# Optimization experiments

Measured on AMD Instinct MI355X. Metric: run time of the kernel, lower is better.

## Reference

```python
import jax, jax.numpy as jnp
import numpy as np

EMBED_DIM = 512
NUM_HEADS = 64
HEAD_DIM = EMBED_DIM // NUM_HEADS  # 8 quantum wires per head
BATCH = 4
SEQ = 1024


def setup_inputs() -> dict:
    key = jax.random.key(0)
    ks = jax.random.split(key, 5)
    s = 1.0 / np.sqrt(EMBED_DIM)
    x = jax.random.normal(ks[0], (BATCH, SEQ, EMBED_DIM), dtype=jnp.float32)
    Wqkv = jax.random.normal(ks[1], (3 * EMBED_DIM, EMBED_DIM), dtype=jnp.float32) * s
    Wout = jax.random.normal(ks[2], (EMBED_DIM, EMBED_DIM), dtype=jnp.float32) * s
    bout = jax.random.normal(ks[3], (EMBED_DIM,), dtype=jnp.float32) * 0.01
    # trainable RX angles, one per (head, wire)
    theta = jax.random.uniform(ks[4], (NUM_HEADS, HEAD_DIM), dtype=jnp.float32,
                               minval=-np.pi, maxval=np.pi)
    return {"x": x, "Wqkv": Wqkv, "Wout": Wout, "bout": bout, "theta": theta}


def _quantum_heads(t, theta):
    # t: [B, H, S, D]; theta: [H, D]
    # Circuit per head: RX(t_i) then RX(theta_i) on wire i (angles add),
    # CNOT chain 0->1->...->D-1, then <Z_j>.
    # Heisenberg: Z_j -> Z_0...Z_j, so <Z_j> = prod_{i<=j} cos(t_i + theta_i).
    c = jnp.cos(t + theta[None, :, None, :])
    return jnp.cumprod(c, axis=-1)


def reference(x, Wqkv, Wout, bout, theta):
    B, S, E = x.shape
    H, D = NUM_HEADS, HEAD_DIM
    qkv = x @ Wqkv.T  # [B, S, 3E]
    q, k, v = jnp.split(qkv, 3, axis=-1)
    sep = lambda t: t.reshape(B, S, H, D).transpose(0, 2, 1, 3)  # [B,H,S,D]
    q, k, v = sep(q), sep(k), sep(v)
    qq = _quantum_heads(q, theta)
    kq = _quantum_heads(k, theta)
    vq = _quantum_heads(v, theta)
    scores = jnp.einsum('bhqd,bhkd->bhqk', qq, kq) / np.sqrt(D)
    probs = jax.nn.softmax(scores, axis=-1)
    attn = jnp.einsum('bhqk,bhkd->bhqd', probs, vq)
    out = attn.transpose(0, 2, 1, 3).reshape(B, S, E)
    return out @ Wout.T + bout
```

## Files before the change

kernel.cpp:

```cpp
#include <hip/hip_runtime.h>

#define SEQ   1024
#define EMBED 512
#define NHEAD 64
#define HDIM  8
#define QPRESCALE 0.5100925247059518f

typedef short bf16x8 __attribute__((ext_vector_type(8)));
typedef float f32x4  __attribute__((ext_vector_type(4)));

union B8 { bf16x8 v; unsigned int u[4]; uint2 u2[2]; };

__device__ __forceinline__ float u2f(unsigned int u) { union { unsigned int u; float f; } c; c.u = u; return c.f; }
__device__ __forceinline__ unsigned int f2u(float f) { union { float f; unsigned int u; } c; c.f = f; return c.u; }
__device__ __forceinline__ unsigned int pk(float e0, float e1) {
    return (f2u(e0) >> 16) | (f2u(e1) & 0xFFFF0000u);
}
__device__ __forceinline__ float tr_hi(float x) { return u2f(f2u(x) & 0xFFFF0000u); }

__global__ __launch_bounds__(256)
void split3_kernel(const float* __restrict__ x, const float* __restrict__ wqkv,
                   const float* __restrict__ wout,
                   unsigned short* __restrict__ xh, unsigned short* __restrict__ xl,
                   unsigned short* __restrict__ wqh, unsigned short* __restrict__ wql,
                   unsigned short* __restrict__ woh, unsigned short* __restrict__ wol)
{
    const int b = blockIdx.x;
    const float* src; unsigned short* hi; unsigned short* lo; int i;
    if (b < 2048)      { src = x;    hi = xh;  lo = xl;  i = b * 256 + threadIdx.x; }
    else if (b < 2816) { src = wqkv; hi = wqh; lo = wql; i = (b - 2048) * 256 + threadIdx.x; }
    else               { src = wout; hi = woh; lo = wol; i = (b - 2816) * 256 + threadIdx.x; }
    const float4 v = ((const float4*)src)[i];
    const float h0 = tr_hi(v.x), h1 = tr_hi(v.y), h2 = tr_hi(v.z), h3 = tr_hi(v.w);
    ((uint2*)hi)[i] = make_uint2(pk(v.x, v.y), pk(v.z, v.w));
    ((uint2*)lo)[i] = make_uint2(pk(v.x - h0, v.y - h1), pk(v.z - h2, v.w - h3));
}

__device__ __forceinline__ void stage_plane(const unsigned short* __restrict__ plane,
                                            int k0, unsigned char* dst, int tid)
{
    const unsigned char* src = (const unsigned char*)plane + k0 * 2;
    #pragma unroll
    for (int p = 0; p < 4; ++p) {
        const int idx = p * 256 + tid;
        const int r = idx >> 3;
        const int q = idx & 7;
        const uint4 v = *(const uint4*)(src + (size_t)r * 1024 + q * 16);
        *(uint4*)(dst + r * 128 + ((q ^ (r & 7)) << 4)) = v;
    }
}

__device__ __forceinline__ void gemm_body_planes(
    const unsigned short* __restrict__ Ahp, const unsigned short* __restrict__ Alp,
    const unsigned short* __restrict__ Bhp, const unsigned short* __restrict__ Blp,
    unsigned char* lds, f32x4 (&acc)[4][4])
{
    unsigned char* Ah = lds;
    unsigned char* Al = lds + 16384;
    unsigned char* Bh = lds + 32768;
    unsigned char* Bl = lds + 49152;
    const int tid  = threadIdx.x;
    const int lane = tid & 63;
    const int w    = tid >> 6;
    const int nw   = (w & 1) * 64;
    const int mw   = (w >> 1) * 64;
    const int col  = lane & 15;
    const int lhi  = lane >> 4;

    for (int k0 = 0; k0 < EMBED; k0 += 64) {
        stage_plane(Ahp, k0, Ah, tid);
        stage_plane(Alp, k0, Al, tid);
        stage_plane(Bhp, k0, Bh, tid);
        stage_plane(Blp, k0, Bl, tid);
        __syncthreads();
        #pragma unroll
        for (int s = 0; s < 2; ++s) {
            bf16x8 ah[4], al[4], bh[4], bl[4];
            #pragma unroll
            for (int j = 0; j < 4; ++j) {
                const int row = nw + j * 16 + col;
                const int addr = row * 128 + (((s * 4 + lhi) ^ (row & 7)) << 4);
                ah[j] = *(const bf16x8*)(Ah + addr);
                al[j] = *(const bf16x8*)(Al + addr);
            }
            #pragma unroll
            for (int i = 0; i < 4; ++i) {
                const int row = mw + i * 16 + col;
                const int addr = row * 128 + (((s * 4 + lhi) ^ (row & 7)) << 4);
                bh[i] = *(const bf16x8*)(Bh + addr);
                bl[i] = *(const bf16x8*)(Bl + addr);
            }
            #pragma unroll
            for (int j = 0; j < 4; ++j)
                #pragma unroll
                for (int i = 0; i < 4; ++i) {
                    acc[j][i] = __builtin_amdgcn_mfma_f32_16x16x32_bf16(ah[j], bh[i], acc[j][i], 0, 0, 0);
                    acc[j][i] = __builtin_amdgcn_mfma_f32_16x16x32_bf16(al[j], bh[i], acc[j][i], 0, 0, 0);
                    acc[j][i] = __builtin_amdgcn_mfma_f32_16x16x32_bf16(ah[j], bl[i], acc[j][i], 0, 0, 0);
                }
        }
        __syncthreads();
    }
}

__global__ __launch_bounds__(256, 2)
void qkv_mfma2_kernel(const unsigned short* __restrict__ xh, const unsigned short* __restrict__ xl,
                      const unsigned short* __restrict__ wqh, const unsigned short* __restrict__ wql,
                      const float* __restrict__ theta,
                      float* __restrict__ qq, float* __restrict__ kq,
                      float* __restrict__ vq)
{
    __shared__ __align__(16) unsigned char lds[65536];
    const int nb = blockIdx.x % 12;
    const int mb = blockIdx.x / 12;
    const int nbase = nb * 128, mbase = mb * 128;

    f32x4 acc[4][4];
    #pragma unroll
    for (int j = 0; j < 4; ++j)
        #pragma unroll
        for (int i = 0; i < 4; ++i) acc[j][i] = (f32x4)(0.f);

    gemm_body_planes(wqh + (size_t)nbase * EMBED, wql + (size_t)nbase * EMBED,
                     xh + (size_t)mbase * EMBED, xl + (size_t)mbase * EMBED, lds, acc);

    const int lane = threadIdx.x & 63;
    const int w    = threadIdx.x >> 6;
    const int nw   = (w & 1) * 64;
    const int mw   = (w >> 1) * 64;
    const int col  = lane & 15;
    const int lhi  = lane >> 4;
    const int dg   = lhi & 1;
    const int seg  = nbase >> 9;
    float* dst     = (seg == 0) ? qq : (seg == 1) ? kq : vq;
    const float qs = (seg == 0) ? QPRESCALE : 1.0f;
    const int nseg0 = (nbase & 511) + nw;

    #pragma unroll
    for (int j = 0; j < 4; ++j) {
        const int nq = nseg0 + j * 16 + lhi * 4;
        const int h  = nq >> 3;
        const float4 th = *(const float4*)(theta + h * 8 + dg * 4);
        #pragma unroll
        for (int i = 0; i < 4; ++i) {
            float p0 = __cosf(acc[j][i][0] + th.x);
            float p1 = p0 * __cosf(acc[j][i][1] + th.y);
            float p2 = p1 * __cosf(acc[j][i][2] + th.z);
            float p3 = p2 * __cosf(acc[j][i][3] + th.w);
            const float tot = __shfl_xor(p3, 16);
            if (dg) { p0 *= tot; p1 *= tot; p2 *= tot; p3 *= tot; }
            const int m = mbase + mw + i * 16 + col;
            const int b = m >> 10, sidx = m & (SEQ - 1);
            float* pdst = dst + (((size_t)(b * NHEAD + h) * SEQ + sidx) << 3) + dg * 4;
            *(float4*)pdst = make_float4(p0 * qs, p1 * qs, p2 * qs, p3 * qs);
        }
    }
}

__global__ __launch_bounds__(256, 2)
void out_mfma2_kernel(const unsigned short* __restrict__ ath, const unsigned short* __restrict__ atl,
                      const unsigned short* __restrict__ woh, const unsigned short* __restrict__ wol,
                      const float* __restrict__ bias, float* __restrict__ out)
{
    __shared__ __align__(16) unsigned char lds[65536];
    const int nb = blockIdx.x & 3;
    const int mb = blockIdx.x >> 2;
    const int nbase = nb * 128, mbase = mb * 128;

    f32x4 acc[4][4];
    #pragma unroll
    for (int j = 0; j < 4; ++j)
        #pragma unroll
        for (int i = 0; i < 4; ++i) acc[j][i] = (f32x4)(0.f);

    gemm_body_planes(woh + (size_t)nbase * EMBED, wol + (size_t)nbase * EMBED,
                     ath + (size_t)mbase * EMBED, atl + (size_t)mbase * EMBED, lds, acc);

    const int lane = threadIdx.x & 63;
    const int w    = threadIdx.x >> 6;
    const int nw   = (w & 1) * 64;
    const int mw   = (w >> 1) * 64;
    const int col  = lane & 15;
    const int lhi  = lane >> 4;

    #pragma unroll
    for (int j = 0; j < 4; ++j) {
        const int n0j = nbase + nw + j * 16 + lhi * 4;
        const float4 bs = *(const float4*)(bias + n0j);
        #pragma unroll
        for (int i = 0; i < 4; ++i) {
            const int m = mbase + mw + i * 16 + col;
            float* p = out + (size_t)m * EMBED + n0j;
            *(float4*)p = make_float4(acc[j][i][0] + bs.x, acc[j][i][1] + bs.y,
                                      acc[j][i][2] + bs.z, acc[j][i][3] + bs.w);
        }
    }
}

__device__ __forceinline__ void stage_tile(const float* __restrict__ src,
                                           unsigned char* hiB, unsigned char* loB,
                                           int tid)
{
    #pragma unroll
    for (int p = 0; p < 8; ++p) {
        const int idx = p * 256 + tid;
        const int r = idx >> 4;
        const int q = idx & 15;
        const float4 v = *(const float4*)(src + (size_t)r * EMBED + q * 4);
        const unsigned int b0 = f2u(v.x), b1 = f2u(v.y), b2 = f2u(v.z), b3 = f2u(v.w);
        const unsigned int h01 = (b0 >> 16) | (b1 & 0xFFFF0000u);
        const unsigned int h23 = (b2 >> 16) | (b3 & 0xFFFF0000u);
        const float r0 = v.x - u2f(b0 & 0xFFFF0000u);
        const float r1 = v.y - u2f(b1 & 0xFFFF0000u);
        const float r2 = v.z - u2f(b2 & 0xFFFF0000u);
        const float r3 = v.w - u2f(b3 & 0xFFFF0000u);
        const unsigned int l01 = (f2u(r0) >> 16) | (f2u(r1) & 0xFFFF0000u);
        const unsigned int l23 = (f2u(r2) >> 16) | (f2u(r3) & 0xFFFF0000u);
        const int addr = r * 128 + (((q >> 1) ^ (r & 7)) << 4) + ((q & 1) << 3);
        *(uint2*)(hiB + addr) = make_uint2(h01, h23);
        *(uint2*)(loB + addr) = make_uint2(l01, l23);
    }
}

__device__ __forceinline__ void gemm_body(const float* __restrict__ A0,
                                          const float* __restrict__ B0,
                                          unsigned char* lds, f32x4 (&acc)[4][4])
{
    unsigned char* Ah = lds;
    unsigned char* Al = lds + 16384;
    unsigned char* Bh = lds + 32768;
    unsigned char* Bl = lds + 49152;
    const int tid  = threadIdx.x;
    const int lane = tid & 63;
    const int w    = tid >> 6;
    const int nw   = (w & 1) * 64;
    const int mw   = (w >> 1) * 64;
    const int col  = lane & 15;
    const int lhi  = lane >> 4;

    for (int k0 = 0; k0 < EMBED; k0 += 64) {
        stage_tile(A0 + k0, Ah, Al, tid);
        stage_tile(B0 + k0, Bh, Bl, tid);
        __syncthreads();
        #pragma unroll
        for (int s = 0; s < 2; ++s) {
            bf16x8 ah[4], al[4], bh[4], bl[4];
            #pragma unroll
            for (int j = 0; j < 4; ++j) {
                const int row = nw + j * 16 + col;
                const int addr = row * 128 + (((s * 4 + lhi) ^ (row & 7)) << 4);
                ah[j] = *(const bf16x8*)(Ah + addr);
                al[j] = *(const bf16x8*)(Al + addr);
            }
            #pragma unroll
            for (int i = 0; i < 4; ++i) {
                const int row = mw + i * 16 + col;
                const int addr = row * 128 + (((s * 4 + lhi) ^ (row & 7)) << 4);
                bh[i] = *(const bf16x8*)(Bh + addr);
                bl[i] = *(const bf16x8*)(Bl + addr);
            }
            #pragma unroll
            for (int j = 0; j < 4; ++j)
                #pragma unroll
                for (int i = 0; i < 4; ++i) {
                    acc[j][i] = __builtin_amdgcn_mfma_f32_16x16x32_bf16(ah[j], bh[i], acc[j][i], 0, 0, 0);
                    acc[j][i] = __builtin_amdgcn_mfma_f32_16x16x32_bf16(al[j], bh[i], acc[j][i], 0, 0, 0);
                    acc[j][i] = __builtin_amdgcn_mfma_f32_16x16x32_bf16(ah[j], bl[i], acc[j][i], 0, 0, 0);
                }
        }
        __syncthreads();
    }
}

__global__ __launch_bounds__(256, 2)
void qkv_mfma_kernel(const float* __restrict__ x, const float* __restrict__ W,
                     const float* __restrict__ theta,
                     float* __restrict__ qq, float* __restrict__ kq,
                     float* __restrict__ vq)
{
    __shared__ __align__(16) unsigned char lds[65536];
    const int nb = blockIdx.x % 12;
    const int mb = blockIdx.x / 12;
    const int nbase = nb * 128, mbase = mb * 128;

    f32x4 acc[4][4];
    #pragma unroll
    for (int j = 0; j < 4; ++j)
        #pragma unroll
        for (int i = 0; i < 4; ++i) acc[j][i] = (f32x4)(0.f);

    gemm_body(W + (size_t)nbase * EMBED, x + (size_t)mbase * EMBED, lds, acc);

    const int lane = threadIdx.x & 63;
    const int w    = threadIdx.x >> 6;
    const int nw   = (w & 1) * 64;
    const int mw   = (w >> 1) * 64;
    const int col  = lane & 15;
    const int lhi  = lane >> 4;
    const int dg   = lhi & 1;
    const int seg  = nbase >> 9;
    float* dst     = (seg == 0) ? qq : (seg == 1) ? kq : vq;
    const float qs = (seg == 0) ? QPRESCALE : 1.0f;
    const int nseg0 = (nbase & 511) + nw;

    #pragma unroll
    for (int j = 0; j < 4; ++j) {
        const int nq = nseg0 + j * 16 + lhi * 4;
        const int h  = nq >> 3;
        const float4 th = *(const float4*)(theta + h * 8 + dg * 4);
        #pragma unroll
        for (int i = 0; i < 4; ++i) {
            float p0 = __cosf(acc[j][i][0] + th.x);
            float p1 = p0 * __cosf(acc[j][i][1] + th.y);
            float p2 = p1 * __cosf(acc[j][i][2] + th.z);
            float p3 = p2 * __cosf(acc[j][i][3] + th.w);
            const float tot = __shfl_xor(p3, 16);
            if (dg) { p0 *= tot; p1 *= tot; p2 *= tot; p3 *= tot; }
            const int m = mbase + mw + i * 16 + col;
            const int b = m >> 10, sidx = m & (SEQ - 1);
            float* pdst = dst + (((size_t)(b * NHEAD + h) * SEQ + sidx) << 3) + dg * 4;
            *(float4*)pdst = make_float4(p0 * qs, p1 * qs, p2 * qs, p3 * qs);
        }
    }
}

__global__ __launch_bounds__(256, 2)
void out_mfma_kernel(const float* __restrict__ A, const float* __restrict__ W,
                     const float* __restrict__ bias, float* __restrict__ out)
{
    __shared__ __align__(16) unsigned char lds[65536];
    const int nb = blockIdx.x & 3;
    const int mb = blockIdx.x >> 2;
    const int nbase = nb * 128, mbase = mb * 128;

    f32x4 acc[4][4];
    #pragma unroll
    for (int j = 0; j < 4; ++j)
        #pragma unroll
        for (int i = 0; i < 4; ++i) acc[j][i] = (f32x4)(0.f);

    gemm_body(W + (size_t)nbase * EMBED, A + (size_t)mbase * EMBED, lds, acc);

    const int lane = threadIdx.x & 63;
    const int w    = threadIdx.x >> 6;
    const int nw   = (w & 1) * 64;
    const int mw   = (w >> 1) * 64;
    const int col  = lane & 15;
    const int lhi  = lane >> 4;

    #pragma unroll
    for (int j = 0; j < 4; ++j) {
        const int n0j = nbase + nw + j * 16 + lhi * 4;
        const float4 bs = *(const float4*)(bias + n0j);
        #pragma unroll
        for (int i = 0; i < 4; ++i) {
            const int m = mbase + mw + i * 16 + col;
            float* p = out + (size_t)m * EMBED + n0j;
            *(float4*)p = make_float4(acc[j][i][0] + bs.x, acc[j][i][1] + bs.y,
                                      acc[j][i][2] + bs.z, acc[j][i][3] + bs.w);
        }
    }
}

template<int PLANES>
__global__ __launch_bounds__(512)
void attn_mfma_kernel(const float* __restrict__ qq, const float* __restrict__ kq,
                      const float* __restrict__ vq, float* __restrict__ attnbuf,
                      unsigned short* __restrict__ ath, unsigned short* __restrict__ atl)
{
    __shared__ __align__(16) unsigned char lds[65536];
    unsigned char* Kh = lds;
    unsigned char* Kl = lds + 16384;
    unsigned char* Vt = lds + 32768;

    const int tid = threadIdx.x;
    const int bh  = blockIdx.x;
    const size_t base = (size_t)bh * SEQ * HDIM;

    #pragma unroll
    for (int p = 0; p < 2; ++p) {
        const int r = tid + p * 512;
        const float4 a = *(const float4*)(kq + base + (size_t)r * 8);
        const float4 b = *(const float4*)(kq + base + (size_t)r * 8 + 4);
        const unsigned int hu0 = pk(a.x, a.y);
        const unsigned int hu1 = pk(a.z, a.w);
        const unsigned int hu2 = pk(b.x, b.y);
        const unsigned int hu3 = pk(b.z, b.w);
        const unsigned int lu0 = pk(a.x - tr_hi(a.x), a.y - tr_hi(a.y));
        const unsigned int lu1 = pk(a.z - tr_hi(a.z), a.w - tr_hi(a.w));
        const unsigned int lu2 = pk(b.x - tr_hi(b.x), b.y - tr_hi(b.y));
        const unsigned int lu3 = pk(b.z - tr_hi(b.z), b.w - tr_hi(b.w));
        *(uint4*)(Kh + r * 16) = make_uint4(hu0, hu1, hu2, hu3);
        *(uint4*)(Kl + r * 16) = make_uint4(lu0, lu1, lu2, lu3);
    }
    {
        const int k0 = tid * 2;
        const float4 va = *(const float4*)(vq + base + (size_t)k0 * 8);
        const float4 vb = *(const float4*)(vq + base + (size_t)k0 * 8 + 4);
        const float4 vc = *(const float4*)(vq + base + (size_t)k0 * 8 + 8);
        const float4 vd = *(const float4*)(vq + base + (size_t)k0 * 8 + 12);
        const float e0[8] = {va.x, va.y, va.z, va.w, vb.x, vb.y, vb.z, vb.w};
        const float e1[8] = {vc.x, vc.y, vc.z, vc.w, vd.x, vd.y, vd.z, vd.w};
        const int blk = k0 >> 3;
        const int byo = (k0 & 7) * 2;
        #pragma unroll
        for (int d = 0; d < 8; ++d) {
            const float h0f = tr_hi(e0[d]), h1f = tr_hi(e1[d]);
            const unsigned int hp = pk(h0f, h1f);
            const unsigned int lp = pk(e0[d] - h0f, e1[d] - h1f);
            const int sb = ((blk ^ (d & 7)) << 4) + byo;
            *(unsigned int*)(Vt + d * 2048 + sb)       = hp;
            *(unsigned int*)(Vt + (d + 8) * 2048 + sb) = lp;
        }
    }
    __syncthreads();

    const int lane = tid & 63;
    const int w    = tid >> 6;
    const int col  = lane & 15;
    const int g    = lane >> 4;
    const int bb   = bh >> 6, hh = bh & 63;
    const int koff = (g >= 2) ? 16384 : 0;
    const int vrowbase = col * 2048;
    const int vswz = (col & 7);

    #pragma unroll 1
    for (int it = 0; it < 8; ++it) {
        const int qrow = (w * 8 + it) * 16 + col;
        const float4 qa = *(const float4*)(qq + base + (size_t)qrow * 8);
        const float4 qb = *(const float4*)(qq + base + (size_t)qrow * 8 + 4);
        B8 qh, ql;
        qh.u[0] = pk(qa.x, qa.y);
        qh.u[1] = pk(qa.z, qa.w);
        qh.u[2] = pk(qb.x, qb.y);
        qh.u[3] = pk(qb.z, qb.w);
        ql.u[0] = pk(qa.x - tr_hi(qa.x), qa.y - tr_hi(qa.y));
        ql.u[1] = pk(qa.z - tr_hi(qa.z), qa.w - tr_hi(qa.w));
        ql.u[2] = pk(qb.x - tr_hi(qb.x), qb.y - tr_hi(qb.y));
        ql.u[3] = pk(qb.z - tr_hi(qb.z), qb.w - tr_hi(qb.w));
        const bf16x8 qfrag = (g & 1) ? ql.v : qh.v;

        f32x4 accO = (f32x4)(0.f);
        float den = 0.f;

        #pragma unroll 2
        for (int ks = 0; ks < 32; ++ks) {
            const bf16x8 ka = *(const bf16x8*)(lds + koff + (size_t)(ks * 32 + col) * 16);
            const bf16x8 kb = *(const bf16x8*)(lds + koff + (size_t)(ks * 32 + 16 + col) * 16);
            f32x4 s0 = __builtin_amdgcn_mfma_f32_16x16x32_bf16(ka, qfrag, (f32x4)(0.f), 0, 0, 0);
            f32x4 s1 = __builtin_amdgcn_mfma_f32_16x16x32_bf16(kb, qfrag, (f32x4)(0.f), 0, 0, 0);
            const float p0 = __builtin_amdgcn_exp2f(s0[0]);
            const float p1 = __builtin_amdgcn_exp2f(s0[1]);
            const float p2 = __builtin_amdgcn_exp2f(s0[2]);
            const float p3 = __builtin_amdgcn_exp2f(s0[3]);
            const float p4 = __builtin_amdgcn_exp2f(s1[0]);
            const float p5 = __builtin_amdgcn_exp2f(s1[1]);
            const float p6 = __builtin_amdgcn_exp2f(s1[2]);
            const float p7 = __builtin_amdgcn_exp2f(s1[3]);
            den += ((p0 + p1) + (p2 + p3)) + ((p4 + p5) + (p6 + p7));
            B8 PH, PL;
            PH.u[0] = pk(p0, p1); PH.u[1] = pk(p2, p3);
            PH.u[2] = pk(p4, p5); PH.u[3] = pk(p6, p7);
            PL.u[0] = pk(p0 - tr_hi(p0), p1 - tr_hi(p1));
            PL.u[1] = pk(p2 - tr_hi(p2), p3 - tr_hi(p3));
            PL.u[2] = pk(p4 - tr_hi(p4), p5 - tr_hi(p5));
            PL.u[3] = pk(p6 - tr_hi(p6), p7 - tr_hi(p7));
            B8 vf;
            const int b0 = ((ks * 4 + (g >> 1)) ^ vswz) * 16 + (g & 1) * 8;
            const int b1 = ((ks * 4 + 2 + (g >> 1)) ^ vswz) * 16 + (g & 1) * 8;
            vf.u2[0] = *(const uint2*)(Vt + vrowbase + b0);
            vf.u2[1] = *(const uint2*)(Vt + vrowbase + b1);
            accO = __builtin_amdgcn_mfma_f32_16x16x32_bf16(vf.v, PH.v, accO, 0, 0, 0);
            accO = __builtin_amdgcn_mfma_f32_16x16x32_bf16(vf.v, PL.v, accO, 0, 0, 0);
        }

        den += __shfl_xor(den, 16);
        den += __shfl_xor(den, 32);
        float o0 = accO[0] + __shfl_xor(accO[0], 32);
        float o1 = accO[1] + __shfl_xor(accO[1], 32);
        float o2 = accO[2] + __shfl_xor(accO[2], 32);
        float o3 = accO[3] + __shfl_xor(accO[3], 32);
        if (g < 2) {
            const float inv = 1.f / den;
            const float s0 = o0 * inv, s1 = o1 * inv, s2 = o2 * inv, s3 = o3 * inv;
            const size_t off = ((size_t)(bb * SEQ + qrow)) * EMBED + hh * 8 + g * 4;
            if (PLANES) {
                const float h0 = tr_hi(s0), h1 = tr_hi(s1), h2 = tr_hi(s2), h3 = tr_hi(s3);
                *(uint2*)(ath + off) = make_uint2(pk(s0, s1), pk(s2, s3));
                *(uint2*)(atl + off) = make_uint2(pk(s0 - h0, s1 - h1), pk(s2 - h2, s3 - h3));
            } else {
                *(float4*)(attnbuf + off) = make_float4(s0, s1, s2, s3);
            }
        }
    }
}

extern "C" void kernel_launch(void* const* d_in, const int* in_sizes, int n_in,
                              void* d_out, int out_size, void* d_ws, size_t ws_size,
                              hipStream_t stream)
{
    const float* x     = (const float*)d_in[0];
    const float* Wqkv  = (const float*)d_in[1];
    const float* Wout  = (const float*)d_in[2];
    const float* bout  = (const float*)d_in[3];
    const float* theta = (const float*)d_in[4];
    float* out = (float*)d_out;

    const size_t per = (size_t)4 * NHEAD * SEQ * HDIM;
    float* qq = (float*)d_ws;
    float* kq = qq + per;
    float* vq = kq + per;

    const size_t NEED = 46137344;
    if (ws_size >= NEED) {
        unsigned short* xh  = (unsigned short*)(vq + per);
        unsigned short* xl  = xh + per;
        unsigned short* wqh = xl + per;
        unsigned short* wql = wqh + 786432;
        unsigned short* woh = wql + 786432;
        unsigned short* wol = woh + 262144;
        unsigned short* ath = wol + 262144;
        unsigned short* atl = ath + per;

        split3_kernel<<<dim3(3072), dim3(256), 0, stream>>>(x, Wqkv, Wout,
                                                            xh, xl, wqh, wql, woh, wol);
        qkv_mfma2_kernel<<<dim3(384), dim3(256), 0, stream>>>(xh, xl, wqh, wql, theta, qq, kq, vq);
        attn_mfma_kernel<1><<<dim3(256), dim3(512), 0, stream>>>(qq, kq, vq, nullptr, ath, atl);
        out_mfma2_kernel<<<dim3(128), dim3(256), 0, stream>>>(ath, atl, woh, wol, bout, out);
    } else {
        float* attnbuf = vq + per;
        qkv_mfma_kernel<<<dim3(384), dim3(256), 0, stream>>>(x, Wqkv, theta, qq, kq, vq);
        attn_mfma_kernel<0><<<dim3(256), dim3(512), 0, stream>>>(qq, kq, vq, attnbuf, nullptr, nullptr);
        out_mfma_kernel<<<dim3(128), dim3(256), 0, stream>>>(attnbuf, Wout, bout, out);
    }
}
```

Before: 184.0 us.

## Split attention query rows across two blocks and drop low-plane P matmul

```diff
diff --git a/kernel.cpp b/kernel.cpp
--- a/kernel.cpp
+++ b/kernel.cpp
@@ -207,15 +207,10 @@
         const int r = idx >> 4;
         const int q = idx & 15;
         const float4 v = *(const float4*)(src + (size_t)r * EMBED + q * 4);
-        const unsigned int b0 = f2u(v.x), b1 = f2u(v.y), b2 = f2u(v.z), b3 = f2u(v.w);
-        const unsigned int h01 = (b0 >> 16) | (b1 & 0xFFFF0000u);
-        const unsigned int h23 = (b2 >> 16) | (b3 & 0xFFFF0000u);
-        const float r0 = v.x - u2f(b0 & 0xFFFF0000u);
-        const float r1 = v.y - u2f(b1 & 0xFFFF0000u);
-        const float r2 = v.z - u2f(b2 & 0xFFFF0000u);
-        const float r3 = v.w - u2f(b3 & 0xFFFF0000u);
-        const unsigned int l01 = (f2u(r0) >> 16) | (f2u(r1) & 0xFFFF0000u);
-        const unsigned int l23 = (f2u(r2) >> 16) | (f2u(r3) & 0xFFFF0000u);
+        const unsigned int h01 = pk(v.x, v.y);
+        const unsigned int h23 = pk(v.z, v.w);
+        const unsigned int l01 = pk(v.x - tr_hi(v.x), v.y - tr_hi(v.y));
+        const unsigned int l23 = pk(v.z - tr_hi(v.z), v.w - tr_hi(v.w));
         const int addr = r * 128 + (((q >> 1) ^ (r & 7)) << 4) + ((q & 1) << 3);
         *(uint2*)(hiB + addr) = make_uint2(h01, h23);
         *(uint2*)(loB + addr) = make_uint2(l01, l23);
@@ -364,9 +359,9 @@
 
 template<int PLANES>
 __global__ __launch_bounds__(512)
-void attn_mfma_kernel(const float* __restrict__ qq, const float* __restrict__ kq,
-                      const float* __restrict__ vq, float* __restrict__ attnbuf,
-                      unsigned short* __restrict__ ath, unsigned short* __restrict__ atl)
+void attn_mfma3_kernel(const float* __restrict__ qq, const float* __restrict__ kq,
+                       const float* __restrict__ vq, float* __restrict__ attnbuf,
+                       unsigned short* __restrict__ ath, unsigned short* __restrict__ atl)
 {
     __shared__ __align__(16) unsigned char lds[65536];
     unsigned char* Kh = lds;
@@ -374,7 +369,8 @@
     unsigned char* Vt = lds + 32768;
 
     const int tid = threadIdx.x;
-    const int bh  = blockIdx.x;
+    const int bh  = blockIdx.x >> 1;
+    const int qh  = blockIdx.x & 1;
     const size_t base = (size_t)bh * SEQ * HDIM;
 
     #pragma unroll
@@ -382,16 +378,13 @@
         const int r = tid + p * 512;
         const float4 a = *(const float4*)(kq + base + (size_t)r * 8);
         const float4 b = *(const float4*)(kq + base + (size_t)r * 8 + 4);
-        const unsigned int hu0 = pk(a.x, a.y);
-        const unsigned int hu1 = pk(a.z, a.w);
-        const unsigned int hu2 = pk(b.x, b.y);
-        const unsigned int hu3 = pk(b.z, b.w);
-        const unsigned int lu0 = pk(a.x - tr_hi(a.x), a.y - tr_hi(a.y));
-        const unsigned int lu1 = pk(a.z - tr_hi(a.z), a.w - tr_hi(a.w));
-        const unsigned int lu2 = pk(b.x - tr_hi(b.x), b.y - tr_hi(b.y));
-        const unsigned int lu3 = pk(b.z - tr_hi(b.z), b.w - tr_hi(b.w));
-        *(uint4*)(Kh + r * 16) = make_uint4(hu0, hu1, hu2, hu3);
-        *(uint4*)(Kl + r * 16) = make_uint4(lu0, lu1, lu2, lu3);
+        *(uint4*)(Kh + r * 16) = make_uint4(pk(a.x, a.y), pk(a.z, a.w),
+                                            pk(b.x, b.y), pk(b.z, b.w));
+        *(uint4*)(Kl + r * 16) = make_uint4(
+            pk(a.x - tr_hi(a.x), a.y - tr_hi(a.y)),
+            pk(a.z - tr_hi(a.z), a.w - tr_hi(a.w)),
+            pk(b.x - tr_hi(b.x), b.y - tr_hi(b.y)),
+            pk(b.z - tr_hi(b.z), b.w - tr_hi(b.w)));
     }
     {
         const int k0 = tid * 2;
@@ -401,16 +394,13 @@
         const float4 vd = *(const float4*)(vq + base + (size_t)k0 * 8 + 12);
         const float e0[8] = {va.x, va.y, va.z, va.w, vb.x, vb.y, vb.z, vb.w};
         const float e1[8] = {vc.x, vc.y, vc.z, vc.w, vd.x, vd.y, vd.z, vd.w};
-        const int blk = k0 >> 3;
-        const int byo = (k0 & 7) * 2;
+        const int sb = (k0 >> 5) * 64 + ((k0 >> 2) & 3) * 16
+                     + ((k0 >> 4) & 1) * 8 + (k0 & 3) * 2;
         #pragma unroll
         for (int d = 0; d < 8; ++d) {
             const float h0f = tr_hi(e0[d]), h1f = tr_hi(e1[d]);
-            const unsigned int hp = pk(h0f, h1f);
-            const unsigned int lp = pk(e0[d] - h0f, e1[d] - h1f);
-            const int sb = ((blk ^ (d & 7)) << 4) + byo;
-            *(unsigned int*)(Vt + d * 2048 + sb)       = hp;
-            *(unsigned int*)(Vt + (d + 8) * 2048 + sb) = lp;
+            *(unsigned int*)(Vt + d * 2048 + sb)       = pk(h0f, h1f);
+            *(unsigned int*)(Vt + (d + 8) * 2048 + sb) = pk(e0[d] - h0f, e1[d] - h1f);
         }
     }
     __syncthreads();
@@ -422,23 +412,20 @@
     const int bb   = bh >> 6, hh = bh & 63;
     const int koff = (g >= 2) ? 16384 : 0;
     const int vrowbase = col * 2048;
-    const int vswz = (col & 7);
 
     #pragma unroll 1
-    for (int it = 0; it < 8; ++it) {
-        const int qrow = (w * 8 + it) * 16 + col;
+    for (int it = 0; it < 4; ++it) {
+        const int qrow = qh * 512 + (w * 4 + it) * 16 + col;
         const float4 qa = *(const float4*)(qq + base + (size_t)qrow * 8);
         const float4 qb = *(const float4*)(qq + base + (size_t)qrow * 8 + 4);
-        B8 qh, ql;
-        qh.u[0] = pk(qa.x, qa.y);
-        qh.u[1] = pk(qa.z, qa.w);
-        qh.u[2] = pk(qb.x, qb.y);
-        qh.u[3] = pk(qb.z, qb.w);
-        ql.u[0] = pk(qa.x - tr_hi(qa.x), qa.y - tr_hi(qa.y));
-        ql.u[1] = pk(qa.z - tr_hi(qa.z), qa.w - tr_hi(qa.w));
-        ql.u[2] = pk(qb.x - tr_hi(qb.x), qb.y - tr_hi(qb.y));
-        ql.u[3] = pk(qb.z - tr_hi(qb.z), qb.w - tr_hi(qb.w));
-        const bf16x8 qfrag = (g & 1) ? ql.v : qh.v;
+        B8 qhf, qlf;
+        qhf.u[0] = pk(qa.x, qa.y);  qhf.u[1] = pk(qa.z, qa.w);
+        qhf.u[2] = pk(qb.x, qb.y);  qhf.u[3] = pk(qb.z, qb.w);
+        qlf.u[0] = pk(qa.x - tr_hi(qa.x), qa.y - tr_hi(qa.y));
+        qlf.u[1] = pk(qa.z - tr_hi(qa.z), qa.w - tr_hi(qa.w));
+        qlf.u[2] = pk(qb.x - tr_hi(qb.x), qb.y - tr_hi(qb.y));
+        qlf.u[3] = pk(qb.z - tr_hi(qb.z), qb.w - tr_hi(qb.w));
+        const bf16x8 qfrag = (g & 1) ? qlf.v : qhf.v;
 
         f32x4 accO = (f32x4)(0.f);
         float den = 0.f;
@@ -458,28 +445,19 @@
             const float p6 = __builtin_amdgcn_exp2f(s1[2]);
             const float p7 = __builtin_amdgcn_exp2f(s1[3]);
             den += ((p0 + p1) + (p2 + p3)) + ((p4 + p5) + (p6 + p7));
-            B8 PH, PL;
+            B8 PH;
             PH.u[0] = pk(p0, p1); PH.u[1] = pk(p2, p3);
             PH.u[2] = pk(p4, p5); PH.u[3] = pk(p6, p7);
-            PL.u[0] = pk(p0 - tr_hi(p0), p1 - tr_hi(p1));
-            PL.u[1] = pk(p2 - tr_hi(p2), p3 - tr_hi(p3));
-            PL.u[2] = pk(p4 - tr_hi(p4), p5 - tr_hi(p5));
-            PL.u[3] = pk(p6 - tr_hi(p6), p7 - tr_hi(p7));
-            B8 vf;
-            const int b0 = ((ks * 4 + (g >> 1)) ^ vswz) * 16 + (g & 1) * 8;
-            const int b1 = ((ks * 4 + 2 + (g >> 1)) ^ vswz) * 16 + (g & 1) * 8;
-            vf.u2[0] = *(const uint2*)(Vt + vrowbase + b0);
-            vf.u2[1] = *(const uint2*)(Vt + vrowbase + b1);
-            accO = __builtin_amdgcn_mfma_f32_16x16x32_bf16(vf.v, PH.v, accO, 0, 0, 0);
-            accO = __builtin_amdgcn_mfma_f32_16x16x32_bf16(vf.v, PL.v, accO, 0, 0, 0);
+            const bf16x8 vf = *(const bf16x8*)(Vt + vrowbase + (ks * 4 + g) * 16);
+            accO = __builtin_amdgcn_mfma_f32_16x16x32_bf16(vf, PH.v, accO, 0, 0, 0);
         }
 
         den += __shfl_xor(den, 16);
         den += __shfl_xor(den, 32);
-        float o0 = accO[0] + __shfl_xor(accO[0], 32);
-        float o1 = accO[1] + __shfl_xor(accO[1], 32);
-        float o2 = accO[2] + __shfl_xor(accO[2], 32);
-        float o3 = accO[3] + __shfl_xor(accO[3], 32);
+        const float o0 = accO[0] + __shfl_xor(accO[0], 32);
+        const float o1 = accO[1] + __shfl_xor(accO[1], 32);
+        const float o2 = accO[2] + __shfl_xor(accO[2], 32);
+        const float o3 = accO[3] + __shfl_xor(accO[3], 32);
         if (g < 2) {
             const float inv = 1.f / den;
             const float s0 = o0 * inv, s1 = o1 * inv, s2 = o2 * inv, s3 = o3 * inv;
@@ -525,12 +503,12 @@
         split3_kernel<<<dim3(3072), dim3(256), 0, stream>>>(x, Wqkv, Wout,
                                                             xh, xl, wqh, wql, woh, wol);
         qkv_mfma2_kernel<<<dim3(384), dim3(256), 0, stream>>>(xh, xl, wqh, wql, theta, qq, kq, vq);
-        attn_mfma_kernel<1><<<dim3(256), dim3(512), 0, stream>>>(qq, kq, vq, nullptr, ath, atl);
+        attn_mfma3_kernel<1><<<dim3(512), dim3(512), 0, stream>>>(qq, kq, vq, nullptr, ath, atl);
         out_mfma2_kernel<<<dim3(128), dim3(256), 0, stream>>>(ath, atl, woh, wol, bout, out);
     } else {
         float* attnbuf = vq + per;
         qkv_mfma_kernel<<<dim3(384), dim3(256), 0, stream>>>(x, Wqkv, theta, qq, kq, vq);
-        attn_mfma_kernel<0><<<dim3(256), dim3(512), 0, stream>>>(qq, kq, vq, attnbuf, nullptr, nullptr);
+        attn_mfma3_kernel<0><<<dim3(512), dim3(512), 0, stream>>>(qq, kq, vq, attnbuf, nullptr, nullptr);
         out_mfma_kernel<<<dim3(128), dim3(256), 0, stream>>>(attnbuf, Wout, bout, out);
     }
 }
```

Result: faster. 163.1 us (-11.4%).
